# Kernel optimization log

Measured on AMD Instinct MI355X. Metric: run time of the kernel, lower is better.

Reference implementation:

```python
import jax, jax.numpy as jnp
import numpy as np

# Constants matching the module's forward-time configuration
NUM_STAGES = 2
HIDDEN_LENGTH = (512, 1024)   # per-stage video token lengths; S = sum = 1536
ENC_LEN = 128                 # text/encoder token length per sample
B, H, D = 8, 16, 64           # batch (interleaved over stages), heads, head_dim
SEQLENS = (np.array([640, 480, 560, 400], np.int32),     # valid lens, stage 0 (Lc=640)
           np.array([1152, 864, 1008, 720], np.int32))   # valid lens, stage 1 (Lc=1152)


def _pack_indices(seqlens, lc):
    return np.concatenate([i * lc + np.arange(l) for i, l in enumerate(seqlens)]).astype(np.int32)


def setup_inputs() -> dict:
    key = jax.random.key(0)
    ks = jax.random.split(key, 6)
    S = sum(HIDDEN_LENGTH)
    inp = {
        'query':         jax.random.normal(ks[0], (B, S, H, D), jnp.float32),
        'key':           jax.random.normal(ks[1], (B, S, H, D), jnp.float32),
        'value':         jax.random.normal(ks[2], (B, S, H, D), jnp.float32),
        'encoder_query': jax.random.normal(ks[3], (B, ENC_LEN, H, D), jnp.float32),
        'encoder_key':   jax.random.normal(ks[4], (B, ENC_LEN, H, D), jnp.float32),
        'encoder_value': jax.random.normal(ks[5], (B, ENC_LEN, H, D), jnp.float32),
        'indices_0': jnp.asarray(_pack_indices(SEQLENS[0], ENC_LEN + HIDDEN_LENGTH[0])),
        'indices_1': jnp.asarray(_pack_indices(SEQLENS[1], ENC_LEN + HIDDEN_LENGTH[1])),
        'seqlens_0': jnp.asarray(SEQLENS[0]),
        'seqlens_1': jnp.asarray(SEQLENS[1]),
        'heads': 16,
        'scale': jnp.asarray(0.125, jnp.float32),  # 1/sqrt(D)
    }
    return inp


def reference(query, key, value, encoder_query, encoder_key, encoder_value,
              indices_0, indices_1, seqlens_0, seqlens_1, heads, scale):
    # Per stage: take the interleaved batch slice, prepend encoder tokens,
    # run non-causal varlen attention (padded + key-masked == flash_attn_varlen),
    # then gather the valid (packed) rows — faithful to index_first_axis packing.
    indices = (indices_0, indices_1)
    seqlens = (seqlens_0, seqlens_1)
    neg = jnp.finfo(query.dtype).min
    outs = []
    i_sum = 0
    for idx, L in enumerate(HIDDEN_LENGTH):
        q_s = jnp.concatenate([encoder_query[idx::NUM_STAGES], query[idx::NUM_STAGES, i_sum:i_sum + L]], axis=1)
        k_s = jnp.concatenate([encoder_key[idx::NUM_STAGES],   key[idx::NUM_STAGES,   i_sum:i_sum + L]], axis=1)
        v_s = jnp.concatenate([encoder_value[idx::NUM_STAGES], value[idx::NUM_STAGES, i_sum:i_sum + L]], axis=1)
        lc = q_s.shape[1]                                    # enc_len + L
        kmask = jnp.arange(lc)[None, :] < seqlens[idx][:, None]   # [b, lc] key validity
        scores = jnp.einsum('bqhd,bkhd->bhqk', q_s, k_s) * scale  # [b,h,lc,lc]
        scores = jnp.where(kmask[:, None, None, :], scores, neg)
        attn = jax.nn.softmax(scores, axis=-1)
        o = jnp.einsum('bhqk,bkhd->bqhd', attn, v_s)              # [b,lc,h,d]
        o_flat = o.reshape(-1, o.shape[2], o.shape[3])            # [(b*lc),h,d]
        outs.append(o_flat[indices[idx]])                          # pack valid rows
        i_sum += L
    return jnp.concatenate(outs, axis=0)  # [total_packed_tokens, H, D]
```

## Files before the change

kernel.cpp:

```cpp
#include <hip/hip_runtime.h>
#include <hip/hip_bf16.h>

typedef __attribute__((ext_vector_type(8))) __bf16 bf16x8;
typedef __attribute__((ext_vector_type(8))) short short8;
typedef __attribute__((ext_vector_type(4))) float f32x4;
typedef __attribute__((ext_vector_type(4))) unsigned int uint4v;

#define KS 72
#define LOG2E 1.44269504088896340736f

__device__ __forceinline__ unsigned pack2bf(float lo, float hi) {
    unsigned a = __builtin_bit_cast(unsigned, lo) + 0x8000u;
    unsigned b = __builtin_bit_cast(unsigned, hi) + 0x8000u;
    return __builtin_amdgcn_perm(b, a, 0x07060302u);
}

__device__ __forceinline__ bf16x8 ldfrag(const short* p) {
    short8 s = *reinterpret_cast<const short8*>(p);
    return __builtin_bit_cast(bf16x8, s);
}

__global__ __launch_bounds__(256, 6) void vfa_kernel(
    const float* __restrict__ qv, const float* __restrict__ kv, const float* __restrict__ vv,
    const float* __restrict__ eq, const float* __restrict__ ek, const float* __restrict__ ev,
    const float* __restrict__ scale_p, float* __restrict__ out)
{
    constexpr int H = 16, Dh = 64, ENC = 128, SV = 1536;
    constexpr int SS_CUM[9] = {0,288,544,768,960,1120,1264,1392,1504};
    constexpr int SEQL[8] = {1152,1008,864,720,640,560,480,400};
    constexpr int QTN[8]  = {18,16,14,12,10,9,8,7};
    constexpr int OB[8]   = {2080,4096,3232,5104,0,1120,640,1680};
    constexpr int BB[8]   = {1,5,3,7,0,4,2,6};
    constexpr int ISUM[8] = {512,512,512,512,0,0,0,0};

    __shared__ __align__(16) short smem[2*64*KS];
    short* kbuf = smem;
    short* vbuf = smem + 64*KS;

    const int bid = blockIdx.x;
    int ss = 0;
    #pragma unroll
    for (int i = 1; i < 8; ++i) ss += (bid >= SS_CUM[i]) ? 1 : 0;
    const int seqlen   = SEQL[ss];
    const int nqt      = QTN[ss];
    const int b        = BB[ss];
    const int isum     = ISUM[ss];
    const int out_base = OB[ss];
    const int local    = bid - SS_CUM[ss];
    const int head     = local / nqt;
    const int qt       = local - head * nqt;

    const int tid  = threadIdx.x;
    const int wave = tid >> 6;
    const int lane = tid & 63;
    const int quad = lane >> 4;
    const int l15  = lane & 15;

    const float qmul = scale_p[0] * LOG2E;

    const int qrow = qt*64 + wave*16 + l15;
    const float* qrp;
    if (qrow < ENC) qrp = eq + ((b*ENC + qrow)*H + head)*Dh;
    else            qrp = qv + (((b*SV + isum) + (qrow - ENC))*H + head)*Dh;
    bf16x8 qfrag[2];
    #pragma unroll
    for (int f = 0; f < 2; ++f) {
        const float* p = qrp + f*32 + quad*8;
        float4 a = *reinterpret_cast<const float4*>(p);
        float4 c = *reinterpret_cast<const float4*>(p + 4);
        uint4v u;
        u[0] = pack2bf(a.x*qmul, a.y*qmul);
        u[1] = pack2bf(a.z*qmul, a.w*qmul);
        u[2] = pack2bf(c.x*qmul, c.y*qmul);
        u[3] = pack2bf(c.z*qmul, c.w*qmul);
        qfrag[f] = __builtin_bit_cast(bf16x8, u);
    }

    f32x4 acc[4];
    #pragma unroll
    for (int dt = 0; dt < 4; ++dt) acc[dt] = {0.f,0.f,0.f,0.f};
    float m_s = -INFINITY, l_s = 0.f;

    const int key_local = tid >> 2;
    const int dbase     = (tid & 3) * 16;
    const int nkt = (seqlen + 63) >> 6;
    const int src_base = l15 + ((quad & 1) << 5);

    for (int kt = 0; kt < nkt; ++kt) {
        if (kt) __syncthreads();
        {
            const int kr = kt*64 + key_local;
            const float *krow, *vrow;
            if (kr < ENC) {
                krow = ek + ((b*ENC + kr)*H + head)*Dh;
                vrow = ev + ((b*ENC + kr)*H + head)*Dh;
            } else {
                const int row = (b*SV + isum) + (kr - ENC);
                krow = kv + (row*H + head)*Dh;
                vrow = vv + (row*H + head)*Dh;
            }
            float4 kf[4], vf[4];
            #pragma unroll
            for (int j = 0; j < 4; ++j) {
                kf[j] = *reinterpret_cast<const float4*>(krow + dbase + 4*j);
                vf[j] = *reinterpret_cast<const float4*>(vrow + dbase + 4*j);
            }
            uint4v kp;
            kp[0] = pack2bf(kf[0].x, kf[0].y);
            kp[1] = pack2bf(kf[0].z, kf[0].w);
            kp[2] = pack2bf(kf[1].x, kf[1].y);
            kp[3] = pack2bf(kf[1].z, kf[1].w);
            *reinterpret_cast<uint4v*>(&kbuf[key_local*KS + dbase]) = kp;
            kp[0] = pack2bf(kf[2].x, kf[2].y);
            kp[1] = pack2bf(kf[2].z, kf[2].w);
            kp[2] = pack2bf(kf[3].x, kf[3].y);
            kp[3] = pack2bf(kf[3].z, kf[3].w);
            *reinterpret_cast<uint4v*>(&kbuf[key_local*KS + dbase + 8]) = kp;
            #pragma unroll
            for (int j = 0; j < 4; ++j) {
                float e[4] = {vf[j].x, vf[j].y, vf[j].z, vf[j].w};
                #pragma unroll
                for (int i = 0; i < 4; ++i) {
                    unsigned u = __builtin_bit_cast(unsigned, e[i]) + 0x8000u;
                    vbuf[(dbase + 4*j + i)*KS + key_local] = (short)(u >> 16);
                }
            }
        }
        __syncthreads();

        const int rem  = seqlen - kt*64;
        const int nsub = (rem >= 64) ? 4 : (rem >> 4);

        float s[4][4];
        #pragma unroll
        for (int sub = 0; sub < 4; ++sub) {
            if (sub < nsub) {
                const short* kr0 = &kbuf[(sub*16 + l15)*KS + quad*8];
                f32x4 sv = {0.f,0.f,0.f,0.f};
                sv = __builtin_amdgcn_mfma_f32_16x16x32_bf16(ldfrag(kr0),      qfrag[0], sv, 0,0,0);
                sv = __builtin_amdgcn_mfma_f32_16x16x32_bf16(ldfrag(kr0 + 32), qfrag[1], sv, 0,0,0);
                #pragma unroll
                for (int r = 0; r < 4; ++r) s[sub][r] = sv[r];
            } else {
                #pragma unroll
                for (int r = 0; r < 4; ++r) s[sub][r] = -INFINITY;
            }
        }

        float mx = s[0][0];
        #pragma unroll
        for (int sub = 0; sub < 4; ++sub)
            #pragma unroll
            for (int r = 0; r < 4; ++r) mx = fmaxf(mx, s[sub][r]);
        mx = fmaxf(mx, __shfl_xor(mx, 16, 64));
        mx = fmaxf(mx, __shfl_xor(mx, 32, 64));
        const float mn = fmaxf(m_s, mx);
        const float alpha = __builtin_amdgcn_exp2f(m_s - mn);
        m_s = mn;
        #pragma unroll
        for (int dt = 0; dt < 4; ++dt)
            #pragma unroll
            for (int r = 0; r < 4; ++r) acc[dt][r] *= alpha;

        float rs = 0.f;
        unsigned pk[4][2];
        #pragma unroll
        for (int sub = 0; sub < 4; ++sub) {
            float p0 = __builtin_amdgcn_exp2f(s[sub][0] - mn);
            float p1 = __builtin_amdgcn_exp2f(s[sub][1] - mn);
            float p2 = __builtin_amdgcn_exp2f(s[sub][2] - mn);
            float p3 = __builtin_amdgcn_exp2f(s[sub][3] - mn);
            rs += (p0 + p1) + (p2 + p3);
            pk[sub][0] = pack2bf(p0, p1);
            pk[sub][1] = pack2bf(p2, p3);
        }
        rs += __shfl_xor(rs, 16, 64);
        rs += __shfl_xor(rs, 32, 64);
        l_s = l_s * alpha + rs;

        #pragma unroll
        for (int kstep = 0; kstep < 2; ++kstep) {
            if (kstep == 0 || nsub > 2) {
                uint4v pf;
                #pragma unroll
                for (int p = 0; p < 4; ++p) {
                    const int sl = src_base + ((p >> 1) << 4);
                    int va = __shfl((int)pk[kstep*2 + 0][p & 1], sl, 64);
                    int vb = __shfl((int)pk[kstep*2 + 1][p & 1], sl, 64);
                    pf[p] = (quad & 2) ? (unsigned)vb : (unsigned)va;
                }
                bf16x8 pfr = __builtin_bit_cast(bf16x8, pf);
                #pragma unroll
                for (int dt = 0; dt < 4; ++dt) {
                    bf16x8 vfr = ldfrag(&vbuf[(dt*16 + l15)*KS + kstep*32 + quad*8]);
                    acc[dt] = __builtin_amdgcn_mfma_f32_16x16x32_bf16(vfr, pfr, acc[dt], 0,0,0);
                }
            }
        }
    }

    __syncthreads();
    float* tbuf = reinterpret_cast<float*>(smem);
    const float inv = 1.0f / l_s;
    #pragma unroll
    for (int dt = 0; dt < 4; ++dt)
        #pragma unroll
        for (int r = 0; r < 4; ++r)
            tbuf[(wave*16 + l15)*68 + dt*16 + quad*4 + r] = acc[dt][r] * inv;
    __syncthreads();

    const int rowl = tid >> 2;
    const int grow = qt*64 + rowl;
    if (grow < seqlen) {
        float* orow = out + (size_t)(out_base + grow)*(H*Dh) + head*Dh;
        const float* trow = tbuf + rowl*68 + (tid & 3)*4;
        #pragma unroll
        for (int c = 0; c < 4; ++c)
            *reinterpret_cast<float4*>(orow + (tid & 3)*4 + c*16) =
                *reinterpret_cast<const float4*>(trow + c*16);
    }
}

extern "C" void kernel_launch(void* const* d_in, const int* in_sizes, int n_in,
                              void* d_out, int out_size, void* d_ws, size_t ws_size,
                              hipStream_t stream) {
    const float* q     = (const float*)d_in[0];
    const float* k     = (const float*)d_in[1];
    const float* v     = (const float*)d_in[2];
    const float* eq    = (const float*)d_in[3];
    const float* ek    = (const float*)d_in[4];
    const float* ev    = (const float*)d_in[5];
    const float* scale = (const float*)d_in[11];
    float* out = (float*)d_out;

    vfa_kernel<<<dim3(1504), dim3(256), 0, stream>>>(q, k, v, eq, ek, ev, scale, out);
}
```

Before: 220.9 us.

## Use 128-row query tiles with 512 threads and double-buffered K/V prefetch

Each block now covers 128 query rows with 8 waves instead of 64 rows with 4 waves. This halves the grid and the number of times each K/V tile is loaded and converted to bf16. The next K/V tile is loaded into registers while the current tile is computed, and the shared-memory buffers are ping-ponged so one barrier per iteration is removed. The LDS row stride changes from 72 to 66; the 16-byte vector LDS accesses then land on addresses that are no longer 16-byte aligned, which risks slower or unsupported accesses. The 512-thread launch bound also tightens register limits.

```diff
diff --git a/kernel.cpp b/kernel.cpp
--- a/kernel.cpp
+++ b/kernel.cpp
@@ -6,7 +6,7 @@
 typedef __attribute__((ext_vector_type(4))) float f32x4;
 typedef __attribute__((ext_vector_type(4))) unsigned int uint4v;
 
-#define KS 72
+#define KS 66
 #define LOG2E 1.44269504088896340736f
 
 __device__ __forceinline__ unsigned pack2bf(float lo, float hi) {
@@ -20,22 +20,20 @@
     return __builtin_bit_cast(bf16x8, s);
 }
 
-__global__ __launch_bounds__(256, 6) void vfa_kernel(
+__global__ __launch_bounds__(512, 6) void vfa_kernel(
     const float* __restrict__ qv, const float* __restrict__ kv, const float* __restrict__ vv,
     const float* __restrict__ eq, const float* __restrict__ ek, const float* __restrict__ ev,
     const float* __restrict__ scale_p, float* __restrict__ out)
 {
     constexpr int H = 16, Dh = 64, ENC = 128, SV = 1536;
-    constexpr int SS_CUM[9] = {0,288,544,768,960,1120,1264,1392,1504};
+    constexpr int SS_CUM[9] = {0,144,272,384,480,560,640,704,768};
     constexpr int SEQL[8] = {1152,1008,864,720,640,560,480,400};
-    constexpr int QTN[8]  = {18,16,14,12,10,9,8,7};
+    constexpr int QTN[8]  = {9,8,7,6,5,5,4,4};
     constexpr int OB[8]   = {2080,4096,3232,5104,0,1120,640,1680};
     constexpr int BB[8]   = {1,5,3,7,0,4,2,6};
     constexpr int ISUM[8] = {512,512,512,512,0,0,0,0};
 
-    __shared__ __align__(16) short smem[2*64*KS];
-    short* kbuf = smem;
-    short* vbuf = smem + 64*KS;
+    __shared__ __align__(16) short smem[2][2*64*KS];
 
     const int bid = blockIdx.x;
     int ss = 0;
@@ -58,7 +56,7 @@
 
     const float qmul = scale_p[0] * LOG2E;
 
-    const int qrow = qt*64 + wave*16 + l15;
+    const int qrow = qt*128 + wave*16 + l15;
     const float* qrp;
     if (qrow < ENC) qrp = eq + ((b*ENC + qrow)*H + head)*Dh;
     else            qrp = qv + (((b*SV + isum) + (qrow - ENC))*H + head)*Dh;
@@ -81,52 +79,54 @@
     for (int dt = 0; dt < 4; ++dt) acc[dt] = {0.f,0.f,0.f,0.f};
     float m_s = -INFINITY, l_s = 0.f;
 
-    const int key_local = tid >> 2;
-    const int dbase     = (tid & 3) * 16;
+    const int kl = tid >> 3;
+    const int g  = tid & 7;
     const int nkt = (seqlen + 63) >> 6;
     const int src_base = l15 + ((quad & 1) << 5);
 
+    float4 kf[2], vf[2];
+    auto load_tile = [&](int kt) {
+        const int kr = kt*64 + kl;
+        const float *krow, *vrow;
+        if (kr < ENC) {
+            krow = ek + ((b*ENC + kr)*H + head)*Dh;
+            vrow = ev + ((b*ENC + kr)*H + head)*Dh;
+        } else {
+            const int row = (b*SV + isum) + (kr - ENC);
+            krow = kv + (row*H + head)*Dh;
+            vrow = vv + (row*H + head)*Dh;
+        }
+        kf[0] = *reinterpret_cast<const float4*>(krow + g*8);
+        kf[1] = *reinterpret_cast<const float4*>(krow + g*8 + 4);
+        vf[0] = *reinterpret_cast<const float4*>(vrow + g*8);
+        vf[1] = *reinterpret_cast<const float4*>(vrow + g*8 + 4);
+    };
+
+    load_tile(0);
+    int p = 0;
+
     for (int kt = 0; kt < nkt; ++kt) {
-        if (kt) __syncthreads();
+        short* kb = smem[p];
+        short* vb = smem[p] + 64*KS;
+
         {
-            const int kr = kt*64 + key_local;
-            const float *krow, *vrow;
-            if (kr < ENC) {
-                krow = ek + ((b*ENC + kr)*H + head)*Dh;
-                vrow = ev + ((b*ENC + kr)*H + head)*Dh;
-            } else {
-                const int row = (b*SV + isum) + (kr - ENC);
-                krow = kv + (row*H + head)*Dh;
-                vrow = vv + (row*H + head)*Dh;
-            }
-            float4 kf[4], vf[4];
-            #pragma unroll
-            for (int j = 0; j < 4; ++j) {
-                kf[j] = *reinterpret_cast<const float4*>(krow + dbase + 4*j);
-                vf[j] = *reinterpret_cast<const float4*>(vrow + dbase + 4*j);
-            }
             uint4v kp;
             kp[0] = pack2bf(kf[0].x, kf[0].y);
             kp[1] = pack2bf(kf[0].z, kf[0].w);
             kp[2] = pack2bf(kf[1].x, kf[1].y);
             kp[3] = pack2bf(kf[1].z, kf[1].w);
-            *reinterpret_cast<uint4v*>(&kbuf[key_local*KS + dbase]) = kp;
-            kp[0] = pack2bf(kf[2].x, kf[2].y);
-            kp[1] = pack2bf(kf[2].z, kf[2].w);
-            kp[2] = pack2bf(kf[3].x, kf[3].y);
-            kp[3] = pack2bf(kf[3].z, kf[3].w);
-            *reinterpret_cast<uint4v*>(&kbuf[key_local*KS + dbase + 8]) = kp;
+            *reinterpret_cast<uint4v*>(&kb[kl*KS + g*8]) = kp;
+            float e[8] = {vf[0].x, vf[0].y, vf[0].z, vf[0].w,
+                          vf[1].x, vf[1].y, vf[1].z, vf[1].w};
             #pragma unroll
-            for (int j = 0; j < 4; ++j) {
-                float e[4] = {vf[j].x, vf[j].y, vf[j].z, vf[j].w};
-                #pragma unroll
-                for (int i = 0; i < 4; ++i) {
-                    unsigned u = __builtin_bit_cast(unsigned, e[i]) + 0x8000u;
-                    vbuf[(dbase + 4*j + i)*KS + key_local] = (short)(u >> 16);
-                }
+            for (int i = 0; i < 8; ++i) {
+                unsigned u = __builtin_bit_cast(unsigned, e[i]) + 0x8000u;
+                vb[(g*8 + i)*KS + kl] = (short)(u >> 16);
             }
         }
         __syncthreads();
+
+        if (kt + 1 < nkt) load_tile(kt + 1);
 
         const int rem  = seqlen - kt*64;
         const int nsub = (rem >= 64) ? 4 : (rem >> 4);
@@ -135,7 +135,7 @@
         #pragma unroll
         for (int sub = 0; sub < 4; ++sub) {
             if (sub < nsub) {
-                const short* kr0 = &kbuf[(sub*16 + l15)*KS + quad*8];
+                const short* kr0 = &kb[(sub*16 + l15)*KS + quad*8];
                 f32x4 sv = {0.f,0.f,0.f,0.f};
                 sv = __builtin_amdgcn_mfma_f32_16x16x32_bf16(ldfrag(kr0),      qfrag[0], sv, 0,0,0);
                 sv = __builtin_amdgcn_mfma_f32_16x16x32_bf16(ldfrag(kr0 + 32), qfrag[1], sv, 0,0,0);
@@ -183,41 +183,42 @@
             if (kstep == 0 || nsub > 2) {
                 uint4v pf;
                 #pragma unroll
-                for (int p = 0; p < 4; ++p) {
-                    const int sl = src_base + ((p >> 1) << 4);
-                    int va = __shfl((int)pk[kstep*2 + 0][p & 1], sl, 64);
-                    int vb = __shfl((int)pk[kstep*2 + 1][p & 1], sl, 64);
-                    pf[p] = (quad & 2) ? (unsigned)vb : (unsigned)va;
+                for (int pp = 0; pp < 4; ++pp) {
+                    const int sl = src_base + ((pp >> 1) << 4);
+                    int va = __shfl((int)pk[kstep*2 + 0][pp & 1], sl, 64);
+                    int vb2 = __shfl((int)pk[kstep*2 + 1][pp & 1], sl, 64);
+                    pf[pp] = (quad & 2) ? (unsigned)vb2 : (unsigned)va;
                 }
                 bf16x8 pfr = __builtin_bit_cast(bf16x8, pf);
                 #pragma unroll
                 for (int dt = 0; dt < 4; ++dt) {
-                    bf16x8 vfr = ldfrag(&vbuf[(dt*16 + l15)*KS + kstep*32 + quad*8]);
+                    bf16x8 vfr = ldfrag(&vb[(dt*16 + l15)*KS + kstep*32 + quad*8]);
                     acc[dt] = __builtin_amdgcn_mfma_f32_16x16x32_bf16(vfr, pfr, acc[dt], 0,0,0);
                 }
             }
         }
+        p ^= 1;
     }
 
     __syncthreads();
-    float* tbuf = reinterpret_cast<float*>(smem);
+    float* tbuf = reinterpret_cast<float*>(&smem[0][0]);
     const float inv = 1.0f / l_s;
     #pragma unroll
     for (int dt = 0; dt < 4; ++dt)
         #pragma unroll
         for (int r = 0; r < 4; ++r)
-            tbuf[(wave*16 + l15)*68 + dt*16 + quad*4 + r] = acc[dt][r] * inv;
+            tbuf[(wave*16 + l15)*66 + dt*16 + quad*4 + r] = acc[dt][r] * inv;
     __syncthreads();
 
     const int rowl = tid >> 2;
-    const int grow = qt*64 + rowl;
+    const int seg  = tid & 3;
+    const int grow = qt*128 + rowl;
     if (grow < seqlen) {
-        float* orow = out + (size_t)(out_base + grow)*(H*Dh) + head*Dh;
-        const float* trow = tbuf + rowl*68 + (tid & 3)*4;
+        float* orow = out + (size_t)(out_base + grow)*(H*Dh) + head*Dh + seg*16;
+        const float* tr = tbuf + rowl*66 + seg*16;
         #pragma unroll
         for (int c = 0; c < 4; ++c)
-            *reinterpret_cast<float4*>(orow + (tid & 3)*4 + c*16) =
-                *reinterpret_cast<const float4*>(trow + c*16);
+            *reinterpret_cast<float4*>(orow + c*4) = *reinterpret_cast<const float4*>(tr + c*4);
     }
 }
 
@@ -233,5 +234,5 @@
     const float* scale = (const float*)d_in[11];
     float* out = (float*)d_out;
 
-    vfa_kernel<<<dim3(1504), dim3(256), 0, stream>>>(q, k, v, eq, ek, ev, scale, out);
-}
+    vfa_kernel<<<dim3(768), dim3(512), 0, stream>>>(q, k, v, eq, ek, ev, scale, out);
+}
```

Result: slower. 341.4 us (+54.5%).
